# Optimization experiments

Hardware: AMD Instinct MI355X
Metric: run time of the kernel (lower is better)

Reference implementation:

```python
import jax, jax.numpy as jnp
import numpy as np
from jax import lax

RATE = 2
KSIZE = 3
FUSE_K = 3
PAD = 1
SCALE = 10.0
ESCAPE_NAN = 1e-4
DN = ('NCHW', 'OIHW', 'NCHW')


def _patches(x, k, s, p):
    # x: [C,H,W] -> [L, C, k, k]  (matches torch pad + unfold(2).unfold(3) + permute)
    C = x.shape[0]
    pt = lax.conv_general_dilated_patches(
        x[None], (k, k), (s, s), [(p, p), (p, p)], dimension_numbers=DN)[0]
    oh, ow = pt.shape[1], pt.shape[2]
    # feature dim ordered (c, kh, kw)
    return pt.reshape(C, k, k, oh * ow).transpose(3, 0, 1, 2)


def setup_inputs() -> dict:
    key = jax.random.key(0)
    k1, k2 = jax.random.split(key)
    f = jax.random.normal(k1, (2, 128, 128, 128), dtype=jnp.float32)
    b = jax.random.normal(k2, (2, 128, 128, 128), dtype=jnp.float32)
    mask = jnp.zeros((1, 1, 128, 128), dtype=jnp.float32)
    return {"f": f, "b": b, "mask": mask}


def reference(f, b, mask):
    B, C, H, W = f.shape
    kernel = 2 * RATE  # 4
    # raw background patches (values for conv_transpose), per sample: [L, C, 4, 4]
    raw_w = jax.vmap(lambda bi: _patches(bi, kernel, RATE, PAD))(b)
    # nearest downsample by rate (torch nearest with scale 1/2 == strided slice)
    fd = f[:, :, ::RATE, ::RATE]
    bd = b[:, :, ::RATE, ::RATE]
    md = mask[:, :, ::RATE, ::RATE]
    fh, fw = fd.shape[2], fd.shape[3]
    bh, bw = bd.shape[2], bd.shape[3]
    L = bh * bw
    # matching (key) patches: [B, L, C, 3, 3]
    w = jax.vmap(lambda bi: _patches(bi, KSIZE, 1, PAD))(bd)
    # mask patches -> mm[l] = 1 where patch mean == 0 (valid background)
    m = _patches(md[0], KSIZE, 1, PAD)           # [L, 1, 3, 3]
    mm = (jnp.mean(m, axis=(1, 2, 3)) == 0.0).astype(f.dtype)[:, None, None]  # [L,1,1]

    fuse_w = jnp.eye(FUSE_K, dtype=f.dtype).reshape(1, 1, FUSE_K, FUSE_K)

    def fuse_conv(y):
        return lax.conv_general_dilated(y, fuse_w, (1, 1), [(1, 1), (1, 1)],
                                        dimension_numbers=DN)

    def one(xi, wi, rwi):
        # xi: [C,fh,fw], wi: [L,C,3,3], rwi: [L,C,4,4]
        norm = jnp.sqrt(jnp.sum(wi * wi, axis=(1, 2, 3), keepdims=True))
        wn = wi / jnp.maximum(norm, ESCAPE_NAN)
        # correlation scores (QK^T analogue): [1, L, fh, fw]
        yi = lax.conv_general_dilated(xi[None], wn, (1, 1), [(1, 1), (1, 1)],
                                      dimension_numbers=DN)
        # diagonal fuse convs, exactly mirroring the torch view/permute sequence
        yi = yi.reshape(1, 1, fh * fw, bh * bw)
        yi = fuse_conv(yi)
        yi = yi.reshape(fh, fw, bh, bw).transpose(1, 0, 3, 2).reshape(1, 1, fh * fw, bh * bw)
        yi = fuse_conv(yi)
        yi = yi.reshape(fw, fh, bw, bh).transpose(1, 0, 3, 2)  # [fh, fw, bh, bw]
        # faithful to the torch .view (plain contiguous reshape, no transpose)
        yi = yi.reshape(bh * bw, fh, fw)
        yi = yi * mm
        yi = jax.nn.softmax(yi * SCALE, axis=0) * mm
        # conv_transpose2d(yi, rwi, stride=rate, padding=1) / 4
        wt = jnp.flip(rwi, axis=(2, 3)).transpose(1, 0, 2, 3)  # [C, L, 4, 4]
        p = kernel - 1 - PAD  # 2
        out = lax.conv_general_dilated(yi[None], wt, (1, 1), [(p, p), (p, p)],
                                       lhs_dilation=(RATE, RATE),
                                       dimension_numbers=DN) / 4.0
        return out[0]  # [C, H, W]

    y = jax.vmap(one)(fd, w, raw_w)  # [B, C, H, W]
    return y
```

## Files before the change

kernel.cpp:

```cpp
#include <hip/hip_runtime.h>

#define CC 128
#define HH 128
#define WW 128
#define DH 64
#define DW 64
#define LTOT 4096
#define K0S 384
#define K2 2048
#define GK 4096
#define GKH 2048
#define SCALE_F 10.0f
#define IMG ((size_t)CC * HH * WW)
#define PSTR 4104

typedef __attribute__((ext_vector_type(8))) short short8;
typedef __attribute__((ext_vector_type(4))) float f32x4;

struct Prep4 { const float* src[4]; unsigned short* dst[4]; float* ssq[4]; int lo[4]; };
struct PtrN2 { const float* ssq[2]; float* invn[2]; float* mmv[2]; };
struct PtrR2 { const float* src[2]; unsigned short* dst[2]; };

__device__ __forceinline__ unsigned short f2bf(float x) {
    union { float f; unsigned u; } v; v.f = x;
    unsigned r = v.u + 0x7fffu + ((v.u >> 16) & 1u);
    return (unsigned short)(r >> 16);
}
__device__ __forceinline__ float bf2f(unsigned short b) {
    union { unsigned u; float f; } v; v.u = ((unsigned)b) << 16;
    return v.f;
}

__device__ __forceinline__ f32x4 ld4u(const float* p) {
    f32x4 r; __builtin_memcpy(&r, p, 16); return r;
}

#define GLDS16(g, l) __builtin_amdgcn_global_load_lds( \
    (const __attribute__((address_space(1))) void*)(g), \
    (__attribute__((address_space(3))) void*)(l), 16, 0, 0)

__global__ __launch_bounds__(128) void split_ds_kernel(Prep4 P) {
    __shared__ float partial[2];
    int z = blockIdx.z;
    const float* __restrict__ src = P.src[z];
    unsigned short* __restrict__ dst = P.dst[z];
    int lo_in_seg1 = P.lo[z];
    int n = blockIdx.x;
    int c = threadIdx.x;
    int ny = n >> 6, nx = n & 63;
    float v = src[((size_t)c * HH + 2 * ny) * WW + 2 * nx];
    unsigned short hi = f2bf(v);
    unsigned short lo = f2bf(v - bf2f(hi));
    unsigned short* drow = dst + (size_t)n * K0S;
    drow[c]       = hi;
    drow[128 + c] = lo_in_seg1 ? lo : hi;
    drow[256 + c] = lo_in_seg1 ? hi : lo;

    float* ssq = P.ssq[z];
    if (ssq) {
        float s2 = v * v;
#pragma unroll
        for (int o = 32; o; o >>= 1) s2 += __shfl_xor(s2, o);
        if ((threadIdx.x & 63) == 0) partial[threadIdx.x >> 6] = s2;
        __syncthreads();
        if (threadIdx.x == 0) ssq[n] = partial[0] + partial[1];
    }
}

__global__ __launch_bounds__(256) void im2col_rawt_kernel(PtrR2 P) {
    int z = blockIdx.z;
    const float* __restrict__ src = P.src[z];
    unsigned short* __restrict__ dst = P.dst[z];
    int idx = blockIdx.x * 256 + threadIdx.x;
    int u  = idx & 31;
    int py = (idx >> 5) & 63;
    int m  = idx >> 11;
    int ke = m & 3, kd = (m >> 2) & 3, c = m >> 4;
    int yy = 2 * py - 1 + kd;
    int xx0 = 4 * u - 1 + ke;
    unsigned short o0 = 0, o1 = 0;
    if (yy >= 0 && yy < HH) {
        const float* row = src + ((size_t)c * HH + yy) * WW;
        if (u == 0 || u == 31) {
            if (xx0 >= 0 && xx0 < WW)         o0 = f2bf(row[xx0]);
            if (xx0 + 2 >= 0 && xx0 + 2 < WW) o1 = f2bf(row[xx0 + 2]);
        } else {
            f32x4 w = ld4u(row + xx0);
            o0 = f2bf(w[0]); o1 = f2bf(w[2]);
        }
    }
    unsigned short* dp = dst + (size_t)m * LTOT + py * 64 + 2 * u;
    dp[0] = o0; dp[1] = o1;
}

__global__ void norm_mm_kernel(PtrN2 P, const float* __restrict__ mask) {
    int z = blockIdx.z;
    const float* __restrict__ ssq = P.ssq[z];
    float* __restrict__ inv_norm = P.invn[z];
    float* __restrict__ mmv = P.mmv[z];
    int p = blockIdx.x * blockDim.x + threadIdx.x;
    int px = p & 63, py = p >> 6;
    float s = 0.f, ms = 0.f;
    for (int di = -1; di <= 1; ++di)
        for (int dj = -1; dj <= 1; ++dj) {
            int y = py + di, x = px + dj;
            if (y >= 0 && y < DH && x >= 0 && x < DW) {
                s += ssq[y * 64 + x];
                ms += mask[(size_t)(2 * y) * WW + 2 * x];
            }
        }
    float n = sqrtf(s);
    if (n < 1e-4f) n = 1e-4f;
    inv_norm[p] = 1.f / n;
    mmv[p] = (ms == 0.f) ? 1.f : 0.f;
}

__global__ __launch_bounds__(256) void gemm_mfma(
    const unsigned short* __restrict__ Aop, const unsigned short* __restrict__ Bop,
    float* __restrict__ C, int M, int N, int K)
{
    __shared__ short As[128 * 64];
    __shared__ short Bs[128 * 64];
    int tid = threadIdx.x;
    int wave = tid >> 6, lane = tid & 63;
    int wm = (wave >> 1) * 64;
    int wn = (wave & 1) * 64;
    int bm = blockIdx.y * 128, bn = blockIdx.x * 128;

    int rowS = wave * 32;
    int lrow8 = lane >> 3;
    int gchunk = ((lane & 7) ^ lrow8) * 8;

    f32x4 acc[4][4] = {};

    int quad = lane >> 4;
    int r16 = lane & 15;
    int pc0 = ((quad)     ^ (r16 & 7)) * 8;
    int pc1 = ((4 + quad) ^ (r16 & 7)) * 8;

    const unsigned short* ap0 = Aop + (size_t)(bm + rowS +  0 + lrow8) * K + gchunk;
    const unsigned short* ap1 = Aop + (size_t)(bm + rowS +  8 + lrow8) * K + gchunk;
    const unsigned short* ap2 = Aop + (size_t)(bm + rowS + 16 + lrow8) * K + gchunk;
    const unsigned short* ap3 = Aop + (size_t)(bm + rowS + 24 + lrow8) * K + gchunk;
    const unsigned short* bp0 = Bop + (size_t)(bn + rowS +  0 + lrow8) * K + gchunk;
    const unsigned short* bp1 = Bop + (size_t)(bn + rowS +  8 + lrow8) * K + gchunk;
    const unsigned short* bp2 = Bop + (size_t)(bn + rowS + 16 + lrow8) * K + gchunk;
    const unsigned short* bp3 = Bop + (size_t)(bn + rowS + 24 + lrow8) * K + gchunk;
    short* lA = As + rowS * 64;
    short* lB = Bs + rowS * 64;

    for (int k0 = 0; k0 < K; k0 += 64) {
        GLDS16(ap0, lA);            GLDS16(ap1, lA + 8 * 64);
        GLDS16(ap2, lA + 16 * 64);  GLDS16(ap3, lA + 24 * 64);
        GLDS16(bp0, lB);            GLDS16(bp1, lB + 8 * 64);
        GLDS16(bp2, lB + 16 * 64);  GLDS16(bp3, lB + 24 * 64);
        ap0 += 64; ap1 += 64; ap2 += 64; ap3 += 64;
        bp0 += 64; bp1 += 64; bp2 += 64; bp3 += 64;
        __syncthreads();

        short8 a0[4], b0[4], a1[4], b1[4];
#pragma unroll
        for (int i = 0; i < 4; ++i) {
            a0[i] = *(const short8*)&As[(wm + i * 16 + r16) * 64 + pc0];
            b0[i] = *(const short8*)&Bs[(wn + i * 16 + r16) * 64 + pc0];
            a1[i] = *(const short8*)&As[(wm + i * 16 + r16) * 64 + pc1];
            b1[i] = *(const short8*)&Bs[(wn + i * 16 + r16) * 64 + pc1];
        }
#pragma unroll
        for (int i = 0; i < 4; ++i)
#pragma unroll
            for (int j = 0; j < 4; ++j) {
                acc[i][j] = __builtin_amdgcn_mfma_f32_16x16x32_bf16(a0[i], b0[j], acc[i][j], 0, 0, 0);
                acc[i][j] = __builtin_amdgcn_mfma_f32_16x16x32_bf16(a1[i], b1[j], acc[i][j], 0, 0, 0);
            }
        __syncthreads();
    }

    int col = lane & 15, rq = (lane >> 4) * 4;
#pragma unroll
    for (int i = 0; i < 4; ++i) {
#pragma unroll
        for (int r = 0; r < 4; ++r) {
            int m = bm + wm + i * 16 + rq + r;
#pragma unroll
            for (int j = 0; j < 4; ++j)
                C[(size_t)m * N + bn + wn + j * 16 + col] = acc[i][j][r];
        }
    }
}

__global__ __launch_bounds__(512, 2) void gemm_k2(
    const unsigned short* __restrict__ Aop, const unsigned short* __restrict__ Bop,
    float* __restrict__ Cpart)
{
    constexpr int NT = 32;
    constexpr int BUFS = 512 * 64;
    __shared__ short lds[2 * BUFS];
    int flat = blockIdx.x;
    int xcd  = flat & 7;
    int slot = (flat >> 3) & 3;
    int bmId = flat >> 5;
    int P    = slot * 8 + xcd;
    int bnId = P >> 1;
    int ks   = P & 1;
    int bm = bmId * 256, bn = bnId * 256;

    int tid = threadIdx.x;
    int wave = tid >> 6, lane = tid & 63;
    int wm = (wave >> 2) * 128;
    int wn = (wave & 3) * 64;
    int lrow8 = lane >> 3;
    int gchunk = ((lane & 7) ^ lrow8) * 8;
    int r16 = lane & 15, quad = lane >> 4;
    int pc0 = ((quad)     ^ (r16 & 7)) * 8;
    int pc1 = ((4 + quad) ^ (r16 & 7)) * 8;

    const size_t ko = (size_t)ks * GKH + gchunk;
    const unsigned short* ap0 = Aop + (size_t)(bm + wave * 32 +  0 + lrow8) * GK + ko;
    const unsigned short* ap1 = Aop + (size_t)(bm + wave * 32 +  8 + lrow8) * GK + ko;
    const unsigned short* ap2 = Aop + (size_t)(bm + wave * 32 + 16 + lrow8) * GK + ko;
    const unsigned short* ap3 = Aop + (size_t)(bm + wave * 32 + 24 + lrow8) * GK + ko;
    const unsigned short* bp0 = Bop + (size_t)(bn + wave * 32 +  0 + lrow8) * GK + ko;
    const unsigned short* bp1 = Bop + (size_t)(bn + wave * 32 +  8 + lrow8) * GK + ko;
    const unsigned short* bp2 = Bop + (size_t)(bn + wave * 32 + 16 + lrow8) * GK + ko;
    const unsigned short* bp3 = Bop + (size_t)(bn + wave * 32 + 24 + lrow8) * GK + ko;

    f32x4 acc[8][4] = {};

#define STAGE2(s) do { \
    short* la = lds + (s) * BUFS + (wave * 32) * 64; \
    short* lb = lds + (s) * BUFS + 256 * 64 + (wave * 32) * 64; \
    GLDS16(ap0, la);            GLDS16(ap1, la + 8 * 64); \
    GLDS16(ap2, la + 16 * 64);  GLDS16(ap3, la + 24 * 64); \
    GLDS16(bp0, lb);            GLDS16(bp1, lb + 8 * 64); \
    GLDS16(bp2, lb + 16 * 64);  GLDS16(bp3, lb + 24 * 64); \
    ap0 += 64; ap1 += 64; ap2 += 64; ap3 += 64; \
    bp0 += 64; bp1 += 64; bp2 += 64; bp3 += 64; } while (0)

    STAGE2(0); STAGE2(1);
    asm volatile("s_waitcnt vmcnt(8)" ::: "memory");
    __builtin_amdgcn_s_barrier();
    asm volatile("" ::: "memory");

    short8 b0[4], b1[4];
    {
        const short* Bb = lds + 256 * 64;
#pragma unroll
        for (int j = 0; j < 4; ++j) {
            b0[j] = *(const short8*)&Bb[(wn + j * 16 + r16) * 64 + pc0];
            b1[j] = *(const short8*)&Bb[(wn + j * 16 + r16) * 64 + pc1];
        }
    }

    int buf = 0;
#pragma unroll 1
    for (int T = 0; T < NT; ++T) {
        const short* Ab = lds + buf * BUFS;
        short8 a0[8], a1[8];
        a0[0] = *(const short8*)&Ab[(wm + r16) * 64 + pc0];
        a1[0] = *(const short8*)&Ab[(wm + r16) * 64 + pc1];
#pragma unroll
        for (int i = 0; i < 8; ++i) {
            if (i < 7) {
                a0[i + 1] = *(const short8*)&Ab[(wm + (i + 1) * 16 + r16) * 64 + pc0];
                a1[i + 1] = *(const short8*)&Ab[(wm + (i + 1) * 16 + r16) * 64 + pc1];
                asm volatile("s_waitcnt lgkmcnt(2)" ::: "memory");
            } else {
                asm volatile("s_waitcnt lgkmcnt(0)" ::: "memory");
            }
            __builtin_amdgcn_sched_barrier(0);
            __builtin_amdgcn_s_setprio(1);
#pragma unroll
            for (int j = 0; j < 4; ++j) {
                acc[i][j] = __builtin_amdgcn_mfma_f32_16x16x32_bf16(a0[i], b0[j], acc[i][j], 0, 0, 0);
                acc[i][j] = __builtin_amdgcn_mfma_f32_16x16x32_bf16(a1[i], b1[j], acc[i][j], 0, 0, 0);
            }
            __builtin_amdgcn_s_setprio(0);
        }
        asm volatile("s_waitcnt vmcnt(0)" ::: "memory");
        __builtin_amdgcn_s_barrier();
        asm volatile("" ::: "memory");
        if (T + 2 < NT) STAGE2(buf);
        if (T + 1 < NT) {
            const short* Bn = lds + (buf ^ 1) * BUFS + 256 * 64;
#pragma unroll
            for (int j = 0; j < 4; ++j) {
                b0[j] = *(const short8*)&Bn[(wn + j * 16 + r16) * 64 + pc0];
                b1[j] = *(const short8*)&Bn[(wn + j * 16 + r16) * 64 + pc1];
            }
        }
        buf ^= 1;
    }
#undef STAGE2

    float* Cout = Cpart + (size_t)ks * K2 * LTOT;
    int col = lane & 15, rq = (lane >> 4) * 4;
#pragma unroll
    for (int i = 0; i < 8; ++i) {
#pragma unroll
        for (int r = 0; r < 4; ++r) {
            int m = bm + wm + i * 16 + rq + r;
#pragma unroll
            for (int j = 0; j < 4; ++j)
                Cout[(size_t)m * LTOT + bn + wn + j * 16 + col] = acc[i][j][r];
        }
    }
}

__global__ __launch_bounds__(256) void stencil_norm_kernel(
    const float* __restrict__ C, const float* __restrict__ invn,
    float* __restrict__ Sg)
{
    int blk = blockIdx.x;
    int q = ((blk & 7) << 9) | (blk >> 3);
    int t = threadIdx.x;
    int qy = q >> 6, qx = q & 63;
    int chunk = t >> 2;
    int lanebase = (t & 3) << 4;
    int p0 = t << 4;

    f32x4 acc[4];
#pragma unroll
    for (int g = 0; g < 4; ++g) { acc[g][0] = acc[g][1] = acc[g][2] = acc[g][3] = 0.f; }

#pragma unroll
    for (int du = -1; du <= 1; ++du) {
        if (qy + du < 0 || qy + du > 63) continue;
        if (chunk + du < 0 || chunk + du > 63) continue;
#pragma unroll
        for (int dv = -1; dv <= 1; ++dv) {
            if (qx + dv < 0 || qx + dv > 63) continue;
            const float* rowp = C + (size_t)(q + 64 * du + dv) * LTOT + 64 * du + dv + p0;
#pragma unroll
            for (int g = 0; g < 4; ++g) {
                f32x4 lv = ld4u(rowp + 4 * g);
                if (dv == -1 && g == 0 && lanebase == 0)  lv[0] = 0.f;
                if (dv ==  1 && g == 3 && lanebase == 48) lv[3] = 0.f;
                acc[g] += lv;
            }
        }
    }
    float* orow = Sg + (size_t)q * PSTR;
#pragma unroll
    for (int g = 0; g < 4; ++g) {
        f32x4 iv = *(const f32x4*)(invn + p0 + 4 * g);
        *(f32x4*)(orow + p0 + 4 * g) = acc[g] * iv;
    }
    if (t == 0) { orow[-4] = orow[-3] = orow[-2] = orow[-1] = 0.f; }
    else if (t == 1) { orow[4096] = orow[4097] = orow[4098] = orow[4099] = 0.f; }
    if (q == 0) {
        float* gr = Sg - 4 - PSTR;
        for (int k = t; k < PSTR; k += 256) gr[k] = 0.f;
    }
    if (q == 4095) {
        float* gr = Sg - 4 + (size_t)4096 * PSTR;
        for (int k = t; k < PSTR; k += 256) gr[k] = 0.f;
    }
}

__global__ __launch_bounds__(256) void fused_conv_softmax_kernel(
    const float* __restrict__ Sg, const float* __restrict__ mmv,
    unsigned short* __restrict__ S16)
{
    __shared__ float redmax[4];
    __shared__ float redsum[4];
    int blk = blockIdx.x;
    int q = ((blk & 7) << 9) | (blk >> 3);
    int t = threadIdx.x;
    int lane = t & 63, wid = t >> 6;
    int chunk = t >> 2;
    int lanebase = (t & 3) << 4;
    int c0 = t << 4;

    int rbase = ((q & 63) << 6) | (q >> 6);

    f32x4 sacc[4];
#pragma unroll
    for (int g = 0; g < 4; ++g) { sacc[g][0] = sacc[g][1] = sacc[g][2] = sacc[g][3] = 0.f; }

#pragma unroll
    for (int j = 0; j < 3; ++j) {
        int r2 = rbase + (j - 1);
        if (r2 < 0 || r2 >= LTOT) continue;
        int rr = ((r2 & 63) << 6) | (r2 >> 6);
        int cj = chunk + (j - 1);
        int ccb;
        if (cj < 0)       ccb = 4031 + lanebase;
        else if (cj > 63) ccb = lanebase + 1;
        else              ccb = (cj << 6) + lanebase;
        const float* pr = Sg + (size_t)rr * PSTR + ccb;
#pragma unroll
        for (int g = 0; g < 4; ++g) {
            const float* pg = pr + 4 * g;
            f32x4 lm = ld4u(pg - (PSTR + 1));
            f32x4 l0 = ld4u(pg);
            f32x4 lp = ld4u(pg + (PSTR + 1));
            f32x4 tj = lm + l0 + lp;
            if (j == 0 && g == 0 && t == 0)   tj[0] = 0.f;
            if (j == 2 && g == 3 && t == 255) tj[3] = 0.f;
            sacc[g] += tj;
        }
    }

    float v[16];
#pragma unroll
    for (int g = 0; g < 4; ++g) {
        f32x4 m4 = *(const f32x4*)(mmv + c0 + 4 * g);
#pragma unroll
        for (int e = 0; e < 4; ++e)
            v[4 * g + e] = sacc[g][e] * m4[e] * SCALE_F;
    }
#pragma unroll
    for (int k = 0; k < 16; ++k) asm volatile("" : "+v"(v[k]));

    float mx = v[0];
#pragma unroll
    for (int i = 1; i < 16; ++i) mx = fmaxf(mx, v[i]);
#pragma unroll
    for (int o = 32; o; o >>= 1) mx = fmaxf(mx, __shfl_xor(mx, o));
    if (lane == 0) redmax[wid] = mx;
    __syncthreads();
    float gmx = fmaxf(fmaxf(redmax[0], redmax[1]), fmaxf(redmax[2], redmax[3]));

    float s = 0.f;
#pragma unroll
    for (int i = 0; i < 16; ++i) {
        v[i] = __expf(v[i] - gmx);
        s += v[i];
    }
#pragma unroll
    for (int o = 32; o; o >>= 1) s += __shfl_xor(s, o);
    if (lane == 0) redsum[wid] = s;
    __syncthreads();
    float inv = 1.f / (redsum[0] + redsum[1] + redsum[2] + redsum[3]);

    unsigned short* orow = S16 + (size_t)q * LTOT + c0;
    short8 h0, h1;
#pragma unroll
    for (int e = 0; e < 8; ++e) {
        h0[e] = (short)f2bf(v[e]     * inv * mmv[c0 + e]);
        h1[e] = (short)f2bf(v[8 + e] * inv * mmv[c0 + 8 + e]);
    }
    *(short8*)orow = h0;
    *(short8*)(orow + 8) = h1;
}

__global__ void output_kernel(const float* __restrict__ C2t, float* __restrict__ out) {
    const float* __restrict__ P1 = C2t + (size_t)K2 * LTOT;
    int idx = blockIdx.x * blockDim.x + threadIdx.x;
    int x = idx & 127;
    int y = (idx >> 7) & 127;
    int c = idx >> 14;
    int oylo = max(0, (y - 1) >> 1), oyhi = min(63, (y + 1) >> 1);
    int oxlo = max(0, (x - 1) >> 1), oxhi = min(63, (x + 1) >> 1);
    float s = 0.f;
    for (int oy = oylo; oy <= oyhi; ++oy)
        for (int ox = oxlo; ox <= oxhi; ++ox) {
            int kd = y - 2 * oy + 1;
            int ke = x - 2 * ox + 1;
            size_t off = (size_t)(c * 16 + kd * 4 + ke) * LTOT + oy * 64 + ox;
            s += C2t[off] + P1[off];
        }
    out[idx] = s * 0.25f;
}

extern "C" void kernel_launch(void* const* d_in, const int* in_sizes, int n_in,
                              void* d_out, int out_size, void* d_ws, size_t ws_size,
                              hipStream_t stream) {
    (void)in_sizes; (void)n_in; (void)out_size; (void)ws_size;
    const float* f    = (const float*)d_in[0];
    const float* b    = (const float*)d_in[1];
    const float* mask = (const float*)d_in[2];
    float* out = (float*)d_out;

    const size_t SZ_MAT  = (size_t)LTOT * LTOT * 4;
    const size_t SZ_SPAD = (size_t)PSTR * 4098 * 4;
    const size_t SZ_WR   = (size_t)K2 * LTOT * 2;
    const size_t SZ_SP   = (size_t)LTOT * K0S * 2;
    const size_t SZ_V    = (size_t)LTOT * 4;

    auto pad = [](size_t n) { return (n + 255) & ~(size_t)255; };
    char* p = (char*)d_ws;
    auto take = [&](size_t n) -> void* { void* r = (void*)p; p += pad(n); return r; };

    take(256);
    float* Buf1 = (float*)take(SZ_MAT);
    float* Spad = (float*)take(SZ_SPAD);
    unsigned short* W = (unsigned short*)take(SZ_WR);
    unsigned short* Bsp0 = (unsigned short*)take(SZ_SP);
    unsigned short* Fsp0 = (unsigned short*)take(SZ_SP);
    unsigned short* Bsp1 = (unsigned short*)take(SZ_SP);
    unsigned short* Fsp1 = (unsigned short*)take(SZ_SP);
    float* ssq0 = (float*)take(SZ_V);  float* ssq1 = (float*)take(SZ_V);
    float* invn0 = (float*)take(SZ_V); float* invn1 = (float*)take(SZ_V);
    float* mmv0 = (float*)take(SZ_V);  float* mmv1 = (float*)take(SZ_V);

    const float* f0 = f,  *b0 = b;
    const float* f1 = f + IMG, *b1 = b + IMG;

    float* Sg = Spad + PSTR + 4;
    unsigned short* S16 = (unsigned short*)Buf1;
    float* C2t = Spad;

    Prep4 P{{b0, f0, b1, f1}, {Bsp0, Fsp0, Bsp1, Fsp1},
            {ssq0, nullptr, ssq1, nullptr}, {1, 0, 1, 0}};
    split_ds_kernel<<<dim3(LTOT, 1, 4), 128, 0, stream>>>(P);
    PtrN2 nm{{ssq0, ssq1}, {invn0, invn1}, {mmv0, mmv1}};
    norm_mm_kernel<<<dim3(16, 1, 2), 256, 0, stream>>>(nm, mask);

    for (int bi = 0; bi < 2; ++bi) {
        const unsigned short* Fsp = bi ? Fsp1 : Fsp0;
        const unsigned short* Bsp = bi ? Bsp1 : Bsp0;
        const float* invn = bi ? invn1 : invn0;
        const float* mmv  = bi ? mmv1 : mmv0;

        PtrR2 rw{{bi ? b1 : b0, nullptr}, {W, nullptr}};
        im2col_rawt_kernel<<<dim3((size_t)K2 * LTOT / 2 / 256, 1, 1), 256, 0, stream>>>(rw);

        gemm_mfma<<<dim3(32, 32), 256, 0, stream>>>(Fsp, Bsp, Buf1, LTOT, LTOT, K0S);

        stencil_norm_kernel<<<LTOT, 256, 0, stream>>>(Buf1, invn, Sg);

        fused_conv_softmax_kernel<<<LTOT, 256, 0, stream>>>(Sg, mmv, S16);

        gemm_k2<<<256, 512, 0, stream>>>(W, S16, C2t);

        output_kernel<<<CC * HH * WW / 256, 256, 0, stream>>>(C2t, out + (size_t)bi * IMG);
    }
}
```

Before: 510.9 us.

## Process multiple rows per block in stencil and softmax kernels; reload B fragments per tile

The stencil-norm kernel now handles four consecutive query rows per block (1024 blocks), and the fused conv-softmax kernel handles two vertically adjacent rows per block (2048 blocks). This is meant to raise per-thread work and memory-level parallelism and to improve cache reuse of overlapping neighbour rows. In the GEMM, the B fragments are now loaded from LDS at the start of each tile iteration rather than prefetched after the barrier, which shortens register lifetime but can expose LDS latency. The extra accumulators raise register pressure and may lower occupancy.

```diff
diff --git a/kernel.cpp b/kernel.cpp
--- a/kernel.cpp
+++ b/kernel.cpp
@@ -242,21 +242,17 @@
     __builtin_amdgcn_s_barrier();
     asm volatile("" ::: "memory");
 
-    short8 b0[4], b1[4];
-    {
-        const short* Bb = lds + 256 * 64;
-#pragma unroll
-        for (int j = 0; j < 4; ++j) {
-            b0[j] = *(const short8*)&Bb[(wn + j * 16 + r16) * 64 + pc0];
-            b1[j] = *(const short8*)&Bb[(wn + j * 16 + r16) * 64 + pc1];
-        }
-    }
-
     int buf = 0;
 #pragma unroll 1
     for (int T = 0; T < NT; ++T) {
         const short* Ab = lds + buf * BUFS;
-        short8 a0[8], a1[8];
+        const short* Bb = Ab + 256 * 64;
+        short8 a0[8], a1[8], b0[4], b1[4];
+#pragma unroll
+        for (int j = 0; j < 4; ++j) {
+            b0[j] = *(const short8*)&Bb[(wn + j * 16 + r16) * 64 + pc0];
+            b1[j] = *(const short8*)&Bb[(wn + j * 16 + r16) * 64 + pc1];
+        }
         a0[0] = *(const short8*)&Ab[(wm + r16) * 64 + pc0];
         a1[0] = *(const short8*)&Ab[(wm + r16) * 64 + pc1];
 #pragma unroll
@@ -281,14 +277,6 @@
         __builtin_amdgcn_s_barrier();
         asm volatile("" ::: "memory");
         if (T + 2 < NT) STAGE2(buf);
-        if (T + 1 < NT) {
-            const short* Bn = lds + (buf ^ 1) * BUFS + 256 * 64;
-#pragma unroll
-            for (int j = 0; j < 4; ++j) {
-                b0[j] = *(const short8*)&Bn[(wn + j * 16 + r16) * 64 + pc0];
-                b1[j] = *(const short8*)&Bn[(wn + j * 16 + r16) * 64 + pc1];
-            }
-        }
         buf ^= 1;
     }
 #undef STAGE2
@@ -312,47 +300,57 @@
     float* __restrict__ Sg)
 {
     int blk = blockIdx.x;
-    int q = ((blk & 7) << 9) | (blk >> 3);
+    int gq = ((blk & 7) << 7) | (blk >> 3);
+    int q0 = gq << 2;
     int t = threadIdx.x;
-    int qy = q >> 6, qx = q & 63;
     int chunk = t >> 2;
     int lanebase = (t & 3) << 4;
     int p0 = t << 4;
 
-    f32x4 acc[4];
-#pragma unroll
-    for (int g = 0; g < 4; ++g) { acc[g][0] = acc[g][1] = acc[g][2] = acc[g][3] = 0.f; }
+    f32x4 acc[4][4];
+#pragma unroll
+    for (int qq = 0; qq < 4; ++qq)
+#pragma unroll
+        for (int g = 0; g < 4; ++g) { acc[qq][g][0] = acc[qq][g][1] = acc[qq][g][2] = acc[qq][g][3] = 0.f; }
 
 #pragma unroll
     for (int du = -1; du <= 1; ++du) {
-        if (qy + du < 0 || qy + du > 63) continue;
         if (chunk + du < 0 || chunk + du > 63) continue;
 #pragma unroll
         for (int dv = -1; dv <= 1; ++dv) {
-            if (qx + dv < 0 || qx + dv > 63) continue;
-            const float* rowp = C + (size_t)(q + 64 * du + dv) * LTOT + 64 * du + dv + p0;
-#pragma unroll
-            for (int g = 0; g < 4; ++g) {
-                f32x4 lv = ld4u(rowp + 4 * g);
-                if (dv == -1 && g == 0 && lanebase == 0)  lv[0] = 0.f;
-                if (dv ==  1 && g == 3 && lanebase == 48) lv[3] = 0.f;
-                acc[g] += lv;
-            }
-        }
-    }
-    float* orow = Sg + (size_t)q * PSTR;
-#pragma unroll
-    for (int g = 0; g < 4; ++g) {
-        f32x4 iv = *(const f32x4*)(invn + p0 + 4 * g);
-        *(f32x4*)(orow + p0 + 4 * g) = acc[g] * iv;
-    }
-    if (t == 0) { orow[-4] = orow[-3] = orow[-2] = orow[-1] = 0.f; }
-    else if (t == 1) { orow[4096] = orow[4097] = orow[4098] = orow[4099] = 0.f; }
-    if (q == 0) {
+#pragma unroll
+            for (int qq = 0; qq < 4; ++qq) {
+                int q = q0 + qq;
+                int qy = q >> 6, qx = q & 63;
+                if (qy + du < 0 || qy + du > 63) continue;
+                if (qx + dv < 0 || qx + dv > 63) continue;
+                const float* rowp = C + (size_t)(q + 64 * du + dv) * LTOT + 64 * du + dv + p0;
+#pragma unroll
+                for (int g = 0; g < 4; ++g) {
+                    f32x4 lv = ld4u(rowp + 4 * g);
+                    if (dv == -1 && g == 0 && lanebase == 0)  lv[0] = 0.f;
+                    if (dv ==  1 && g == 3 && lanebase == 48) lv[3] = 0.f;
+                    acc[qq][g] += lv;
+                }
+            }
+        }
+    }
+#pragma unroll
+    for (int qq = 0; qq < 4; ++qq) {
+        float* orow = Sg + (size_t)(q0 + qq) * PSTR;
+#pragma unroll
+        for (int g = 0; g < 4; ++g) {
+            f32x4 iv = *(const f32x4*)(invn + p0 + 4 * g);
+            *(f32x4*)(orow + p0 + 4 * g) = acc[qq][g] * iv;
+        }
+        if (t == 0) { orow[-4] = orow[-3] = orow[-2] = orow[-1] = 0.f; }
+        else if (t == 1) { orow[4096] = orow[4097] = orow[4098] = orow[4099] = 0.f; }
+    }
+    if (q0 == 0) {
         float* gr = Sg - 4 - PSTR;
         for (int k = t; k < PSTR; k += 256) gr[k] = 0.f;
     }
-    if (q == 4095) {
+    if (q0 == 4092) {
         float* gr = Sg - 4 + (size_t)4096 * PSTR;
         for (int k = t; k < PSTR; k += 256) gr[k] = 0.f;
     }
@@ -362,87 +360,114 @@
     const float* __restrict__ Sg, const float* __restrict__ mmv,
     unsigned short* __restrict__ S16)
 {
-    __shared__ float redmax[4];
-    __shared__ float redsum[4];
+    __shared__ float redmax[8];
+    __shared__ float redsum[8];
     int blk = blockIdx.x;
-    int q = ((blk & 7) << 9) | (blk >> 3);
+    int h = ((blk & 7) << 8) | (blk >> 3);
+    int qx = h & 63, qy2 = h >> 6;
+    int qA = (2 * qy2) * 64 + qx;
+    int qB = qA + 64;
     int t = threadIdx.x;
     int lane = t & 63, wid = t >> 6;
     int chunk = t >> 2;
     int lanebase = (t & 3) << 4;
     int c0 = t << 4;
 
-    int rbase = ((q & 63) << 6) | (q >> 6);
-
-    f32x4 sacc[4];
-#pragma unroll
-    for (int g = 0; g < 4; ++g) { sacc[g][0] = sacc[g][1] = sacc[g][2] = sacc[g][3] = 0.f; }
+    int rbA = ((qA & 63) << 6) | (qA >> 6);
+    int rbB = rbA + 1;
+
+    f32x4 sA[4], sB[4];
+#pragma unroll
+    for (int g = 0; g < 4; ++g) {
+        sA[g][0] = sA[g][1] = sA[g][2] = sA[g][3] = 0.f;
+        sB[g][0] = sB[g][1] = sB[g][2] = sB[g][3] = 0.f;
+    }
 
 #pragma unroll
     for (int j = 0; j < 3; ++j) {
-        int r2 = rbase + (j - 1);
-        if (r2 < 0 || r2 >= LTOT) continue;
-        int rr = ((r2 & 63) << 6) | (r2 >> 6);
         int cj = chunk + (j - 1);
         int ccb;
         if (cj < 0)       ccb = 4031 + lanebase;
         else if (cj > 63) ccb = lanebase + 1;
         else              ccb = (cj << 6) + lanebase;
-        const float* pr = Sg + (size_t)rr * PSTR + ccb;
-#pragma unroll
-        for (int g = 0; g < 4; ++g) {
-            const float* pg = pr + 4 * g;
-            f32x4 lm = ld4u(pg - (PSTR + 1));
-            f32x4 l0 = ld4u(pg);
-            f32x4 lp = ld4u(pg + (PSTR + 1));
-            f32x4 tj = lm + l0 + lp;
-            if (j == 0 && g == 0 && t == 0)   tj[0] = 0.f;
-            if (j == 2 && g == 3 && t == 255) tj[3] = 0.f;
-            sacc[g] += tj;
-        }
-    }
-
-    float v[16];
+
+        int r2A = rbA + (j - 1);
+        if (r2A >= 0 && r2A < LTOT) {
+            int rr = ((r2A & 63) << 6) | ((r2A >> 6) & 63);
+            const float* pr = Sg + (size_t)rr * PSTR + ccb;
+#pragma unroll
+            for (int g = 0; g < 4; ++g) {
+                const float* pg = pr + 4 * g;
+                f32x4 tj = ld4u(pg - (PSTR + 1)) + ld4u(pg) + ld4u(pg + (PSTR + 1));
+                if (j == 0 && g == 0 && t == 0)   tj[0] = 0.f;
+                if (j == 2 && g == 3 && t == 255) tj[3] = 0.f;
+                sA[g] += tj;
+            }
+        }
+        int r2B = rbB + (j - 1);
+        if (r2B >= 0 && r2B < LTOT) {
+            int rr = ((r2B & 63) << 6) | ((r2B >> 6) & 63);
+            const float* pr = Sg + (size_t)rr * PSTR + ccb;
+#pragma unroll
+            for (int g = 0; g < 4; ++g) {
+                const float* pg = pr + 4 * g;
+                f32x4 tj = ld4u(pg - (PSTR + 1)) + ld4u(pg) + ld4u(pg + (PSTR + 1));
+                if (j == 0 && g == 0 && t == 0)   tj[0] = 0.f;
+                if (j == 2 && g == 3 && t == 255) tj[3] = 0.f;
+                sB[g] += tj;
+            }
+        }
+    }
+
+    float vA[16], vB[16];
 #pragma unroll
     for (int g = 0; g < 4; ++g) {
         f32x4 m4 = *(const f32x4*)(mmv + c0 + 4 * g);
 #pragma unroll
-        for (int e = 0; e < 4; ++e)
-            v[4 * g + e] = sacc[g][e] * m4[e] * SCALE_F;
-    }
-#pragma unroll
-    for (int k = 0; k < 16; ++k) asm volatile("" : "+v"(v[k]));
-
-    float mx = v[0];
-#pragma unroll
-    for (int i = 1; i < 16; ++i) mx = fmaxf(mx, v[i]);
-#pragma unroll
-    for (int o = 32; o; o >>= 1) mx = fmaxf(mx, __shfl_xor(mx, o));
-    if (lane == 0) redmax[wid] = mx;
+        for (int e = 0; e < 4; ++e) {
+            vA[4 * g + e] = sA[g][e] * m4[e] * SCALE_F;
+            vB[4 * g + e] = sB[g][e] * m4[e] * SCALE_F;
+        }
+    }
+#pragma unroll
+    for (int k = 0; k < 16; ++k) { asm volatile("" : "+v"(vA[k])); asm volatile("" : "+v"(vB[k])); }
+
+    float mxA = vA[0], mxB = vB[0];
+#pragma unroll
+    for (int i = 1; i < 16; ++i) { mxA = fmaxf(mxA, vA[i]); mxB = fmaxf(mxB, vB[i]); }
+#pragma unroll
+    for (int o = 32; o; o >>= 1) { mxA = fmaxf(mxA, __shfl_xor(mxA, o)); mxB = fmaxf(mxB, __shfl_xor(mxB, o)); }
+    if (lane == 0) { redmax[wid] = mxA; redmax[4 + wid] = mxB; }
     __syncthreads();
-    float gmx = fmaxf(fmaxf(redmax[0], redmax[1]), fmaxf(redmax[2], redmax[3]));
-
-    float s = 0.f;
+    float gmxA = fmaxf(fmaxf(redmax[0], redmax[1]), fmaxf(redmax[2], redmax[3]));
+    float gmxB = fmaxf(fmaxf(redmax[4], redmax[5]), fmaxf(redmax[6], redmax[7]));
+
+    float suA = 0.f, suB = 0.f;
 #pragma unroll
     for (int i = 0; i < 16; ++i) {
-        v[i] = __expf(v[i] - gmx);
-        s += v[i];
-    }
-#pragma unroll
-    for (int o = 32; o; o >>= 1) s += __shfl_xor(s, o);
-    if (lane == 0) redsum[wid] = s;
+        vA[i] = __expf(vA[i] - gmxA); suA += vA[i];
+        vB[i] = __expf(vB[i] - gmxB); suB += vB[i];
+    }
+#pragma unroll
+    for (int o = 32; o; o >>= 1) { suA += __shfl_xor(suA, o); suB += __shfl_xor(suB, o); }
+    if (lane == 0) { redsum[wid] = suA; redsum[4 + wid] = suB; }
     __syncthreads();
-    float inv = 1.f / (redsum[0] + redsum[1] + redsum[2] + redsum[3]);
-
-    unsigned short* orow = S16 + (size_t)q * LTOT + c0;
-    short8 h0, h1;
+    float invA = 1.f / (redsum[0] + redsum[1] + redsum[2] + redsum[3]);
+    float invB = 1.f / (redsum[4] + redsum[5] + redsum[6] + redsum[7]);
+
+    unsigned short* orowA = S16 + (size_t)qA * LTOT + c0;
+    unsigned short* orowB = S16 + (size_t)qB * LTOT + c0;
+    short8 hA0, hA1, hB0, hB1;
 #pragma unroll
     for (int e = 0; e < 8; ++e) {
-        h0[e] = (short)f2bf(v[e]     * inv * mmv[c0 + e]);
-        h1[e] = (short)f2bf(v[8 + e] * inv * mmv[c0 + 8 + e]);
-    }
-    *(short8*)orow = h0;
-    *(short8*)(orow + 8) = h1;
+        float m0 = mmv[c0 + e], m1 = mmv[c0 + 8 + e];
+        hA0[e] = (short)f2bf(vA[e]     * invA * m0);
+        hA1[e] = (short)f2bf(vA[8 + e] * invA * m1);
+        hB0[e] = (short)f2bf(vB[e]     * invB * m0);
+        hB1[e] = (short)f2bf(vB[8 + e] * invB * m1);
+    }
+    *(short8*)orowA = hA0; *(short8*)(orowA + 8) = hA1;
+    *(short8*)orowB = hB0; *(short8*)(orowB + 8) = hB1;
 }
 
 __global__ void output_kernel(const float* __restrict__ C2t, float* __restrict__ out) {
@@ -519,9 +544,9 @@
 
         gemm_mfma<<<dim3(32, 32), 256, 0, stream>>>(Fsp, Bsp, Buf1, LTOT, LTOT, K0S);
 
-        stencil_norm_kernel<<<LTOT, 256, 0, stream>>>(Buf1, invn, Sg);
-
-        fused_conv_softmax_kernel<<<LTOT, 256, 0, stream>>>(Sg, mmv, S16);
+        stencil_norm_kernel<<<1024, 256, 0, stream>>>(Buf1, invn, Sg);
+
+        fused_conv_softmax_kernel<<<2048, 256, 0, stream>>>(Sg, mmv, S16);
 
         gemm_k2<<<256, 512, 0, stream>>>(W, S16, C2t);
 
```

Result: slower. 549.7 us (+7.6%).
